# Performance work log

Measured on AMD Instinct MI355X. Metric: run time of the kernel, lower is better.

## Reference

```python
import jax, jax.numpy as jnp
import numpy as np

DIM = 1024
NUM_HEADS = 16
HEAD_DIM = DIM // NUM_HEADS
B, L = 4, 2048


def setup_inputs() -> dict:
    key = jax.random.key(0)
    ks = jax.random.split(key, 9)
    s = 0.02
    return {
        "x": jax.random.normal(ks[0], (B, L, DIM), jnp.float32),
        "Wq": jax.random.normal(ks[1], (DIM, DIM), jnp.float32) * s,
        "bq": jax.random.normal(ks[2], (DIM,), jnp.float32) * s,
        "Wk": jax.random.normal(ks[3], (DIM, DIM), jnp.float32) * s,
        "bk": jax.random.normal(ks[4], (DIM,), jnp.float32) * s,
        "Wv": jax.random.normal(ks[5], (DIM, DIM), jnp.float32) * s,
        "bv": jax.random.normal(ks[6], (DIM,), jnp.float32) * s,
        "Wo": jax.random.normal(ks[7], (DIM, DIM), jnp.float32) * s,
        "bo": jax.random.normal(ks[8], (DIM,), jnp.float32) * s,
    }


def _alibi_bias_causal(seq_len, dtype):
    # slopes m_h = 2^(-8h/H), h = 1..H
    h = jnp.arange(1, NUM_HEADS + 1, dtype=jnp.float32)
    slopes = jnp.power(2.0, -8.0 * h / NUM_HEADS)  # [H]
    pos = jnp.arange(seq_len, dtype=jnp.float32)
    rel = jnp.abs(pos[:, None] - pos[None, :])  # [L, L]
    bias = -slopes[:, None, None] * rel[None, :, :]  # [H, L, L]
    causal = pos[:, None] >= pos[None, :]  # lower-triangular True
    bias = jnp.where(causal[None, :, :], bias, -jnp.inf)
    return bias.astype(dtype)  # [H, L, L]


def reference(x, Wq, bq, Wk, bk, Wv, bv, Wo, bo):
    b, l, d = x.shape
    # torch Linear: y = x @ W.T + b
    q = (jnp.einsum('bld,ed->ble', x, Wq) + bq).reshape(b, l, NUM_HEADS, HEAD_DIM).transpose(0, 2, 1, 3)
    k = (jnp.einsum('bld,ed->ble', x, Wk) + bk).reshape(b, l, NUM_HEADS, HEAD_DIM).transpose(0, 2, 1, 3)
    v = (jnp.einsum('bld,ed->ble', x, Wv) + bv).reshape(b, l, NUM_HEADS, HEAD_DIM).transpose(0, 2, 1, 3)

    scale = 1.0 / np.sqrt(HEAD_DIM)
    scores = jnp.einsum('bhqd,bhkd->bhqk', q, k) * scale  # [B,H,L,L]
    scores = scores + _alibi_bias_causal(l, scores.dtype)[None]  # causal -inf inside bias
    attn = jax.nn.softmax(scores, axis=-1)
    out = jnp.einsum('bhqk,bhkd->bhqd', attn, v)  # [B,H,L,hd]
    out = out.transpose(0, 2, 1, 3).reshape(b, l, d)
    return jnp.einsum('bld,ed->ble', out, Wo) + bo
```

## Files before the change

kernel.cpp:

```cpp
#include <hip/hip_runtime.h>
#include <hip/hip_bf16.h>

typedef __bf16 bf16;
typedef __attribute__((ext_vector_type(4))) __bf16 bf16x4;
typedef __attribute__((ext_vector_type(8))) __bf16 bf16x8;
typedef __attribute__((ext_vector_type(4))) float f32x4;

#define MFMA16(a,b,c) __builtin_amdgcn_mfma_f32_16x16x32_bf16((a),(b),(c),0,0,0)

constexpr int BSZ = 4, SEQ = 2048, DIM = 1024, NH = 16, HD = 64;
constexpr long SZ    = (long)BSZ * SEQ * DIM;
constexpr long BSLOT = (long)SEQ * DIM;
constexpr long WSZ   = (long)DIM * DIM;

__device__ inline bf16x8 ld8(const bf16* p) { return *(const bf16x8*)p; }
__device__ inline bf16x8 ld8(const float* p) {
    f32x4 a = *(const f32x4*)p;
    f32x4 b = *(const f32x4*)(p + 4);
    bf16x8 r;
    r[0] = (bf16)a[0]; r[1] = (bf16)a[1]; r[2] = (bf16)a[2]; r[3] = (bf16)a[3];
    r[4] = (bf16)b[0]; r[5] = (bf16)b[1]; r[6] = (bf16)b[2]; r[7] = (bf16)b[3];
    return r;
}

__device__ inline void async16(const bf16* g, bf16* l) {
    __builtin_amdgcn_global_load_lds(
        (const __attribute__((address_space(1))) unsigned int*)g,
        (__attribute__((address_space(3))) unsigned int*)l,
        16, 0, 0);
}

__global__ __launch_bounds__(256) void cvt1(const float* __restrict__ s,
                                            bf16* __restrict__ d, long n) {
    const long i = ((long)blockIdx.x * 256 + threadIdx.x) * 8;
    if (i < n) *(bf16x8*)(d + i) = ld8(s + i);
}
__global__ __launch_bounds__(256) void cvt4(
    const float* __restrict__ x,  const float* __restrict__ Wq,
    const float* __restrict__ Wk, const float* __restrict__ Wv,
    bf16* __restrict__ xb, bf16* __restrict__ wqb,
    bf16* __restrict__ wkb, bf16* __restrict__ wvb) {
    const long i = ((long)blockIdx.x * 256 + threadIdx.x) * 8;
    const float* s; bf16* d; long off;
    if (i < SZ) { s = x; d = xb; off = i; }
    else {
        const long j = i - SZ;
        const int w = (int)(j >> 20);
        off = j & (WSZ - 1);
        s = (w == 0) ? Wq : (w == 1) ? Wk : Wv;
        d = (w == 0) ? wqb : (w == 1) ? wkb : wvb;
    }
    *(bf16x8*)(d + off) = ld8(s + off);
}

template <typename CT>
__global__ __launch_bounds__(256) void gemm_bb(
    const bf16* __restrict__ A,
    const bf16* __restrict__ W0, const bf16* __restrict__ W1, const bf16* __restrict__ W2,
    const float* __restrict__ b0, const float* __restrict__ b1, const float* __restrict__ b2,
    CT* __restrict__ C0, CT* __restrict__ C1, CT* __restrict__ C2,
    int M, int N, int K)
{
    const int z = blockIdx.z;
    const bf16* W     = (z == 0) ? W0 : ((z == 1) ? W1 : W2);
    const float* bias = (z == 0) ? b0 : ((z == 1) ? b1 : b2);
    CT* C             = (z == 0) ? C0 : ((z == 1) ? C1 : C2);

    __shared__ __align__(16) bf16 As[2][128][32];
    __shared__ __align__(16) bf16 Bs[2][128][32];

    const int tid  = threadIdx.x;
    const int lane = tid & 63;
    const int wave = tid >> 6;
    const int l15  = lane & 15;
    const int quad = lane >> 4;

    const int m0 = blockIdx.x * 128;
    const int n0 = blockIdx.y * 128;
    const int wm = (wave >> 1) * 64;
    const int wn = (wave & 1) * 64;

    f32x4 acc[4][4];
#pragma unroll
    for (int i = 0; i < 4; i++)
#pragma unroll
        for (int j = 0; j < 4; j++) acc[i][j] = f32x4{0.f, 0.f, 0.f, 0.f};

    const int r1 = tid >> 2,         c1 = (tid & 3) * 8;
    const int r2 = (tid + 256) >> 2, c2 = ((tid + 256) & 3) * 8;

    async16(A + (long)(m0 + r1) * K + c1, &As[0][r1][c1]);
    async16(A + (long)(m0 + r2) * K + c2, &As[0][r2][c2]);
    async16(W + (long)(n0 + r1) * K + c1, &Bs[0][r1][c1]);
    async16(W + (long)(n0 + r2) * K + c2, &Bs[0][r2][c2]);
    __syncthreads();

    const int NT = K >> 5;
    for (int t = 0; t < NT; t++) {
        const int cur = t & 1;
        if (t + 1 < NT) {
            const int k0 = (t + 1) * 32;
            async16(A + (long)(m0 + r1) * K + k0 + c1, &As[cur ^ 1][r1][c1]);
            async16(A + (long)(m0 + r2) * K + k0 + c2, &As[cur ^ 1][r2][c2]);
            async16(W + (long)(n0 + r1) * K + k0 + c1, &Bs[cur ^ 1][r1][c1]);
            async16(W + (long)(n0 + r2) * K + k0 + c2, &Bs[cur ^ 1][r2][c2]);
        }

        bf16x8 af[4], bfr[4];
#pragma unroll
        for (int t4 = 0; t4 < 4; t4++) {
            af[t4]  = *(const bf16x8*)&As[cur][wm + t4 * 16 + l15][quad * 8];
            bfr[t4] = *(const bf16x8*)&Bs[cur][wn + t4 * 16 + l15][quad * 8];
        }
#pragma unroll
        for (int i = 0; i < 4; i++)
#pragma unroll
            for (int j = 0; j < 4; j++)
                acc[i][j] = MFMA16(af[i], bfr[j], acc[i][j]);

        __syncthreads();
    }

#pragma unroll
    for (int j = 0; j < 4; j++) {
        const float bv = bias[n0 + wn + j * 16 + l15];
        const long col = n0 + wn + j * 16 + l15;
#pragma unroll
        for (int i = 0; i < 4; i++) {
            const long row = m0 + wm + i * 16 + quad * 4;
#pragma unroll
            for (int r = 0; r < 4; r++)
                C[(row + r) * N + col] = (CT)(acc[i][j][r] + bv);
        }
    }
}

template <typename AT, typename CT>
__global__ __launch_bounds__(256) void gemm_bt(
    const AT* __restrict__ A,
    const float* __restrict__ W0, const float* __restrict__ W1, const float* __restrict__ W2,
    const float* __restrict__ b0, const float* __restrict__ b1, const float* __restrict__ b2,
    CT* __restrict__ C0, CT* __restrict__ C1, CT* __restrict__ C2,
    int M, int N, int K)
{
    const int z = blockIdx.z;
    const float* W    = (z == 0) ? W0 : ((z == 1) ? W1 : W2);
    const float* bias = (z == 0) ? b0 : ((z == 1) ? b1 : b2);
    CT* C             = (z == 0) ? C0 : ((z == 1) ? C1 : C2);

    __shared__ __align__(16) bf16 As[128][32];
    __shared__ __align__(16) bf16 Bs[128][32];

    const int tid  = threadIdx.x;
    const int lane = tid & 63;
    const int wave = tid >> 6;
    const int l15  = lane & 15;
    const int quad = lane >> 4;

    const int m0 = blockIdx.x * 128;
    const int n0 = blockIdx.y * 128;
    const int wm = (wave >> 1) * 64;
    const int wn = (wave & 1) * 64;

    f32x4 acc[4][4];
#pragma unroll
    for (int i = 0; i < 4; i++)
#pragma unroll
        for (int j = 0; j < 4; j++) acc[i][j] = f32x4{0.f, 0.f, 0.f, 0.f};

    const int r1 = tid >> 2,         c1 = (tid & 3) * 8;
    const int r2 = (tid + 256) >> 2, c2 = ((tid + 256) & 3) * 8;

    for (int k0 = 0; k0 < K; k0 += 32) {
        __syncthreads();
        *(bf16x8*)&As[r1][c1] = ld8(A + (long)(m0 + r1) * K + k0 + c1);
        *(bf16x8*)&As[r2][c2] = ld8(A + (long)(m0 + r2) * K + k0 + c2);
        *(bf16x8*)&Bs[r1][c1] = ld8(W + (long)(n0 + r1) * K + k0 + c1);
        *(bf16x8*)&Bs[r2][c2] = ld8(W + (long)(n0 + r2) * K + k0 + c2);
        __syncthreads();

        bf16x8 af[4], bfr[4];
#pragma unroll
        for (int t = 0; t < 4; t++) {
            af[t]  = *(const bf16x8*)&As[wm + t * 16 + l15][quad * 8];
            bfr[t] = *(const bf16x8*)&Bs[wn + t * 16 + l15][quad * 8];
        }
#pragma unroll
        for (int i = 0; i < 4; i++)
#pragma unroll
            for (int j = 0; j < 4; j++)
                acc[i][j] = MFMA16(af[i], bfr[j], acc[i][j]);
    }

#pragma unroll
    for (int j = 0; j < 4; j++) {
        const float bv = bias[n0 + wn + j * 16 + l15];
        const long col = n0 + wn + j * 16 + l15;
#pragma unroll
        for (int i = 0; i < 4; i++) {
            const long row = m0 + wm + i * 16 + quad * 4;
#pragma unroll
            for (int r = 0; r < 4; r++)
                C[(row + r) * N + col] = (CT)(acc[i][j][r] + bv);
        }
    }
}

__global__ __launch_bounds__(256, 4) void attn(
    const bf16* __restrict__ Kw, const bf16* __restrict__ Vw,
    bf16* __restrict__ QOw)
{
    const int z  = blockIdx.y;
    const int bh = blockIdx.x;
    const int b = bh >> 4, h = bh & 15;
    const int qtA = z, qtB = 31 - z;
    const int tid = threadIdx.x, wave = tid >> 6, lane = tid & 63;
    const int l15 = lane & 15, quad = lane >> 4;

    __shared__ __align__(16) bf16 Vt[2][64][72];
    __shared__ __align__(16) bf16 Kt[2][64][64];
    __shared__ __align__(16) bf16 Pl[2][4][16][72];

    const long base = (long)b * SEQ * DIM + h * HD;
    const int q0A = qtA * 64 + wave * 16;
    const int q0B = qtB * 64 + wave * 16;

    bf16x8 qA0, qA1, qB0, qB1;
    {
        const bf16* pA = QOw + base + (long)(q0A + l15) * DIM + quad * 8;
        qA0 = *(const bf16x8*)pA; qA1 = *(const bf16x8*)(pA + 32);
        const bf16* pB = QOw + base + (long)(q0B + l15) * DIM + quad * 8;
        qB0 = *(const bf16x8*)pB; qB1 = *(const bf16x8*)(pB + 32);
    }

    constexpr float LOG2E = 1.4426950408889634f;
    const float slope = exp2f(-0.5f * (float)(h + 1));
    const float c1 = 0.125f * LOG2E;
    const float ns = slope * LOG2E;
    const float MC = 16.0f * LOG2E;

    float lrA = 0.f, lrB = 0.f;
    f32x4 oA[4], oB[4];
#pragma unroll
    for (int d = 0; d < 4; d++) { oA[d] = f32x4{0,0,0,0}; oB[d] = f32x4{0,0,0,0}; }

    const int sk0 = tid >> 3,         sd0 = (tid & 7) * 8;
    const int sk1 = (tid + 256) >> 3, sd1 = ((tid + 256) & 7) * 8;
    const int vc0 = sk0 ^ sd0,        vc1 = sk1 ^ sd1;

    auto stageK = [&](int kt, int bi) {
#pragma unroll
        for (int t = 0; t < 2; t++) {
            const int s = tid + 256 * t;
            const int r = s >> 3, u = s & 7;
            const int gc = (u ^ (r & 7)) * 8;
            async16(Kw + base + (long)(kt * 64 + r) * DIM + gc, &Kt[bi][r][u * 8]);
        }
    };

    stageK(0, 0);
    {
        bf16x8 v0 = *(const bf16x8*)(Vw + base + (long)sk0 * DIM + sd0);
        bf16x8 v1 = *(const bf16x8*)(Vw + base + (long)sk1 * DIM + sd1);
#pragma unroll
        for (int i = 0; i < 8; i++) Vt[0][sd0 + i][vc0] = v0[i];
#pragma unroll
        for (int i = 0; i < 8; i++) Vt[0][sd1 + i][vc1] = v1[i];
    }
    __syncthreads();

    const int klq = quad * 4;
    const int qlB = wave * 16 + l15;
    const int kc0 = (quad ^ (l15 & 7)) * 8;

    for (int kt = 0; kt <= qtB; kt++) {
        const int bi = kt & 1;
        const bool more = (kt < qtB);
        const bool dual = (kt <= qtA);

        bf16x8 vn0, vn1;
        if (more) {
            stageK(kt + 1, bi ^ 1);
            vn0 = *(const bf16x8*)(Vw + base + (long)((kt + 1) * 64 + sk0) * DIM + sd0);
            vn1 = *(const bf16x8*)(Vw + base + (long)((kt + 1) * 64 + sk1) * DIM + sd1);
        }

        f32x4 sB[4], sA[4];
#pragma unroll
        for (int nt = 0; nt < 4; nt++) {
            const int row = nt * 16 + l15;
            bf16x8 k0 = *(const bf16x8*)&Kt[bi][row][kc0];
            bf16x8 k1 = *(const bf16x8*)&Kt[bi][row][kc0 ^ 32];
            f32x4 a = f32x4{0,0,0,0};
            a = MFMA16(k0, qB0, a); a = MFMA16(k1, qB1, a);
            sB[nt] = a;
            if (dual) {
                f32x4 c = f32x4{0,0,0,0};
                c = MFMA16(k0, qA0, c); c = MFMA16(k1, qA1, c);
                sA[nt] = c;
            }
        }

        {
            const float t0 = fmaf(ns, (float)(kt * 64 + klq - q0B - l15), -MC);
            const bool diag = (kt == qtB);
#pragma unroll
            for (int nt = 0; nt < 4; nt++) {
                const float bn = fmaf(ns, (float)(16 * nt), t0);
                bf16x4 p4;
#pragma unroll
                for (int r = 0; r < 4; r++) {
                    float arg = fmaf(sB[nt][r], c1, fmaf(ns, (float)r, bn));
                    if (diag && (nt * 16 + klq + r > qlB)) arg = -1e30f;
                    const float p = exp2f(arg);
                    lrB += p;
                    p4[r] = (bf16)p;
                }
                *(bf16x4*)&Pl[0][wave][l15][nt * 16 + klq] = p4;
            }
        }

        if (dual) {
            const float t0 = fmaf(ns, (float)(kt * 64 + klq - q0A - l15), -MC);
            const bool diag = (kt == qtA);
#pragma unroll
            for (int nt = 0; nt < 4; nt++) {
                const float bn = fmaf(ns, (float)(16 * nt), t0);
                bf16x4 p4;
#pragma unroll
                for (int r = 0; r < 4; r++) {
                    float arg = fmaf(sA[nt][r], c1, fmaf(ns, (float)r, bn));
                    if (diag && (nt * 16 + klq + r > qlB)) arg = -1e30f;
                    const float p = exp2f(arg);
                    lrA += p;
                    p4[r] = (bf16)p;
                }
                *(bf16x4*)&Pl[1][wave][l15][nt * 16 + klq] = p4;
            }
        } else if (more) {
#pragma unroll
            for (int i = 0; i < 8; i++) Vt[bi ^ 1][sd0 + i][vc0] = vn0[i];
#pragma unroll
            for (int i = 0; i < 8; i++) Vt[bi ^ 1][sd1 + i][vc1] = vn1[i];
        }

        {
            bf16x8 p0 = *(const bf16x8*)&Pl[0][wave][l15][quad * 8];
            bf16x8 p1 = *(const bf16x8*)&Pl[0][wave][l15][32 + quad * 8];
#pragma unroll
            for (int dt = 0; dt < 4; dt++) {
                const int d = dt * 16 + l15;
                const int c0 = (quad * 8) ^ (d & 56);
                bf16x8 v0 = *(const bf16x8*)&Vt[bi][d][c0];
                bf16x8 v1 = *(const bf16x8*)&Vt[bi][d][c0 ^ 32];
                oB[dt] = MFMA16(p0, v0, oB[dt]);
                oB[dt] = MFMA16(p1, v1, oB[dt]);
            }
        }

        if (dual) {
            bf16x8 p0 = *(const bf16x8*)&Pl[1][wave][l15][quad * 8];
            bf16x8 p1 = *(const bf16x8*)&Pl[1][wave][l15][32 + quad * 8];
#pragma unroll
            for (int dt = 0; dt < 4; dt++) {
                const int d = dt * 16 + l15;
                const int c0 = (quad * 8) ^ (d & 56);
                bf16x8 v0 = *(const bf16x8*)&Vt[bi][d][c0];
                bf16x8 v1 = *(const bf16x8*)&Vt[bi][d][c0 ^ 32];
                oA[dt] = MFMA16(p0, v0, oA[dt]);
                oA[dt] = MFMA16(p1, v1, oA[dt]);
            }
#pragma unroll
            for (int i = 0; i < 8; i++) Vt[bi ^ 1][sd0 + i][vc0] = vn0[i];
#pragma unroll
            for (int i = 0; i < 8; i++) Vt[bi ^ 1][sd1 + i][vc1] = vn1[i];
        }
        __syncthreads();
    }

    lrB += __shfl_xor(lrB, 16, 64); lrB += __shfl_xor(lrB, 32, 64);
    lrA += __shfl_xor(lrA, 16, 64); lrA += __shfl_xor(lrA, 32, 64);
#pragma unroll
    for (int r = 0; r < 4; r++) {
        const float ivB = 1.0f / __shfl(lrB, quad * 4 + r, 64);
        const float ivA = 1.0f / __shfl(lrA, quad * 4 + r, 64);
        const long rwB = q0B + quad * 4 + r;
        const long rwA = q0A + quad * 4 + r;
#pragma unroll
        for (int dt = 0; dt < 4; dt++) {
            QOw[base + rwB * DIM + dt * 16 + l15] = (bf16)(oB[dt][r] * ivB);
            QOw[base + rwA * DIM + dt * 16 + l15] = (bf16)(oA[dt][r] * ivA);
        }
    }
}

extern "C" void kernel_launch(void* const* d_in, const int* in_sizes, int n_in,
                              void* d_out, int out_size, void* d_ws, size_t ws_size,
                              hipStream_t stream)
{
    const float* x  = (const float*)d_in[0];
    const float* Wq = (const float*)d_in[1];
    const float* bq = (const float*)d_in[2];
    const float* Wk = (const float*)d_in[3];
    const float* bk = (const float*)d_in[4];
    const float* Wv = (const float*)d_in[5];
    const float* bv = (const float*)d_in[6];
    const float* Wo = (const float*)d_in[7];
    const float* bo = (const float*)d_in[8];
    float* out = (float*)d_out;

    dim3 blk(256, 1, 1);

    if (ws_size >= (size_t)SZ * sizeof(bf16)) {
        bf16* xb  = (bf16*)d_out;
        bf16* Wqb = xb + SZ;
        bf16* Wkb = Wqb + WSZ;
        bf16* Wvb = Wkb + WSZ;
        bf16* Qb  = (bf16*)d_ws;
        bf16* Kb  = (bf16*)d_in[0];
        bf16* Vb  = Kb + SZ;
        bf16* Wob = Kb;

        cvt4<<<dim3(5632, 1, 1), blk, 0, stream>>>(x, Wq, Wk, Wv, xb, Wqb, Wkb, Wvb);

        dim3 g1(64, 8, 3);
        gemm_bb<bf16><<<g1, blk, 0, stream>>>(xb, Wqb, Wkb, Wvb, bq, bk, bv,
                                              Qb, Kb, Vb, BSZ * SEQ, DIM, DIM);
        dim3 g2(BSZ * NH, 16, 1);
        attn<<<g2, blk, 0, stream>>>(Kb, Vb, Qb);

        cvt1<<<dim3(512, 1, 1), blk, 0, stream>>>(Wo, Wob, WSZ);

        dim3 g3(64, 8, 1);
        gemm_bb<float><<<g3, blk, 0, stream>>>(Qb, Wob, Wob, Wob, bo, bo, bo,
                                               out, out, out, BSZ * SEQ, DIM, DIM);
    } else {
        bf16* outB = (bf16*)d_out;
        float* xm = const_cast<float*>(x);
        bf16* x0a = (bf16*)xm;
        bf16* x0b = x0a + BSLOT;
        bf16* x1a = (bf16*)(xm + BSLOT);

        bf16* Qs[4] = { outB + 2 * BSLOT, x0a, x0a, x0a };
        bf16* Ks[4] = { outB + 3 * BSLOT, x0b, x0b, x0b };
        bf16* Vs[4] = { outB + 4 * BSLOT, outB + 6 * BSLOT, x1a, x1a };

        dim3 gqkv(SEQ / 128, DIM / 128, 3);
        dim3 gattn(NH, 16, 1);
        dim3 gproj(SEQ / 128, DIM / 128, 1);

        for (int b = 0; b < 4; b++) {
            gemm_bt<float, bf16><<<gqkv, blk, 0, stream>>>(x + b * BSLOT, Wq, Wk, Wv,
                                                           bq, bk, bv,
                                                           Qs[b], Ks[b], Vs[b], SEQ, DIM, DIM);
            attn<<<gattn, blk, 0, stream>>>(Ks[b], Vs[b], Qs[b]);
            gemm_bt<bf16, float><<<gproj, blk, 0, stream>>>(Qs[b], Wo, Wo, Wo, bo, bo, bo,
                                                            out + b * BSLOT, out + b * BSLOT,
                                                            out + b * BSLOT, SEQ, DIM, DIM);
        }
    }
}
```

Measured before the change: 285.4 us.

## Single-buffer V and P tiles in attention, fold Wo conversion into first cast kernel

The attention kernel drops the double-buffered V tile and the second P staging buffer. Each branch now computes its P tile and immediately runs the PV MFMAs, and the next V tile is written after an extra barrier. This cuts LDS use per block, which may allow more resident blocks, at the cost of an additional __syncthreads per iteration and less overlap of V staging with compute. Separately, when the workspace is large enough, Wo is converted to bf16 together with x/Wq/Wk/Wv in one launch, removing the separate cvt1 launch.

```diff
diff --git a/kernel.cpp b/kernel.cpp
--- a/kernel.cpp
+++ b/kernel.cpp
@@ -52,6 +52,25 @@
     }
     *(bf16x8*)(d + off) = ld8(s + off);
 }
+__global__ __launch_bounds__(256) void cvt5(
+    const float* __restrict__ x,  const float* __restrict__ Wq,
+    const float* __restrict__ Wk, const float* __restrict__ Wv,
+    const float* __restrict__ Wo,
+    bf16* __restrict__ xb, bf16* __restrict__ wqb,
+    bf16* __restrict__ wkb, bf16* __restrict__ wvb,
+    bf16* __restrict__ wob) {
+    const long i = ((long)blockIdx.x * 256 + threadIdx.x) * 8;
+    const float* s; bf16* d; long off;
+    if (i < SZ) { s = x; d = xb; off = i; }
+    else {
+        const long j = i - SZ;
+        const int w = (int)(j >> 20);
+        off = j & (WSZ - 1);
+        s = (w == 0) ? Wq : (w == 1) ? Wk : (w == 2) ? Wv : Wo;
+        d = (w == 0) ? wqb : (w == 1) ? wkb : (w == 2) ? wvb : wob;
+    }
+    *(bf16x8*)(d + off) = ld8(s + off);
+}
 
 template <typename CT>
 __global__ __launch_bounds__(256) void gemm_bb(
@@ -217,9 +236,9 @@
     const int tid = threadIdx.x, wave = tid >> 6, lane = tid & 63;
     const int l15 = lane & 15, quad = lane >> 4;
 
-    __shared__ __align__(16) bf16 Vt[2][64][72];
+    __shared__ __align__(16) bf16 Vt[64][72];
     __shared__ __align__(16) bf16 Kt[2][64][64];
-    __shared__ __align__(16) bf16 Pl[2][4][16][72];
+    __shared__ __align__(16) bf16 Pl[4][16][72];
 
     const long base = (long)b * SEQ * DIM + h * HD;
     const int q0A = qtA * 64 + wave * 16;
@@ -263,9 +282,9 @@
         bf16x8 v0 = *(const bf16x8*)(Vw + base + (long)sk0 * DIM + sd0);
         bf16x8 v1 = *(const bf16x8*)(Vw + base + (long)sk1 * DIM + sd1);
 #pragma unroll
-        for (int i = 0; i < 8; i++) Vt[0][sd0 + i][vc0] = v0[i];
-#pragma unroll
-        for (int i = 0; i < 8; i++) Vt[0][sd1 + i][vc1] = v1[i];
+        for (int i = 0; i < 8; i++) Vt[sd0 + i][vc0] = v0[i];
+#pragma unroll
+        for (int i = 0; i < 8; i++) Vt[sd1 + i][vc1] = v1[i];
     }
     __syncthreads();
 
@@ -316,7 +335,21 @@
                     lrB += p;
                     p4[r] = (bf16)p;
                 }
-                *(bf16x4*)&Pl[0][wave][l15][nt * 16 + klq] = p4;
+                *(bf16x4*)&Pl[wave][l15][nt * 16 + klq] = p4;
+            }
+        }
+
+        {
+            bf16x8 p0 = *(const bf16x8*)&Pl[wave][l15][quad * 8];
+            bf16x8 p1 = *(const bf16x8*)&Pl[wave][l15][32 + quad * 8];
+#pragma unroll
+            for (int dt = 0; dt < 4; dt++) {
+                const int d = dt * 16 + l15;
+                const int c0 = (quad * 8) ^ (d & 56);
+                bf16x8 v0 = *(const bf16x8*)&Vt[d][c0];
+                bf16x8 v1 = *(const bf16x8*)&Vt[d][c0 ^ 32];
+                oB[dt] = MFMA16(p0, v0, oB[dt]);
+                oB[dt] = MFMA16(p1, v1, oB[dt]);
             }
         }
 
@@ -335,47 +368,29 @@
                     lrA += p;
                     p4[r] = (bf16)p;
                 }
-                *(bf16x4*)&Pl[1][wave][l15][nt * 16 + klq] = p4;
+                *(bf16x4*)&Pl[wave][l15][nt * 16 + klq] = p4;
             }
-        } else if (more) {
-#pragma unroll
-            for (int i = 0; i < 8; i++) Vt[bi ^ 1][sd0 + i][vc0] = vn0[i];
-#pragma unroll
-            for (int i = 0; i < 8; i++) Vt[bi ^ 1][sd1 + i][vc1] = vn1[i];
-        }
-
-        {
-            bf16x8 p0 = *(const bf16x8*)&Pl[0][wave][l15][quad * 8];
-            bf16x8 p1 = *(const bf16x8*)&Pl[0][wave][l15][32 + quad * 8];
+            bf16x8 p0 = *(const bf16x8*)&Pl[wave][l15][quad * 8];
+            bf16x8 p1 = *(const bf16x8*)&Pl[wave][l15][32 + quad * 8];
 #pragma unroll
             for (int dt = 0; dt < 4; dt++) {
                 const int d = dt * 16 + l15;
                 const int c0 = (quad * 8) ^ (d & 56);
-                bf16x8 v0 = *(const bf16x8*)&Vt[bi][d][c0];
-                bf16x8 v1 = *(const bf16x8*)&Vt[bi][d][c0 ^ 32];
-                oB[dt] = MFMA16(p0, v0, oB[dt]);
-                oB[dt] = MFMA16(p1, v1, oB[dt]);
-            }
-        }
-
-        if (dual) {
-            bf16x8 p0 = *(const bf16x8*)&Pl[1][wave][l15][quad * 8];
-            bf16x8 p1 = *(const bf16x8*)&Pl[1][wave][l15][32 + quad * 8];
-#pragma unroll
-            for (int dt = 0; dt < 4; dt++) {
-                const int d = dt * 16 + l15;
-                const int c0 = (quad * 8) ^ (d & 56);
-                bf16x8 v0 = *(const bf16x8*)&Vt[bi][d][c0];
-                bf16x8 v1 = *(const bf16x8*)&Vt[bi][d][c0 ^ 32];
+                bf16x8 v0 = *(const bf16x8*)&Vt[d][c0];
+                bf16x8 v1 = *(const bf16x8*)&Vt[d][c0 ^ 32];
                 oA[dt] = MFMA16(p0, v0, oA[dt]);
                 oA[dt] = MFMA16(p1, v1, oA[dt]);
             }
-#pragma unroll
-            for (int i = 0; i < 8; i++) Vt[bi ^ 1][sd0 + i][vc0] = vn0[i];
-#pragma unroll
-            for (int i = 0; i < 8; i++) Vt[bi ^ 1][sd1 + i][vc1] = vn1[i];
-        }
+        }
+
         __syncthreads();
+        if (more) {
+#pragma unroll
+            for (int i = 0; i < 8; i++) Vt[sd0 + i][vc0] = vn0[i];
+#pragma unroll
+            for (int i = 0; i < 8; i++) Vt[sd1 + i][vc1] = vn1[i];
+            __syncthreads();
+        }
     }
 
     lrB += __shfl_xor(lrB, 16, 64); lrB += __shfl_xor(lrB, 32, 64);
@@ -419,9 +434,17 @@
         bf16* Qb  = (bf16*)d_ws;
         bf16* Kb  = (bf16*)d_in[0];
         bf16* Vb  = Kb + SZ;
-        bf16* Wob = Kb;
-
-        cvt4<<<dim3(5632, 1, 1), blk, 0, stream>>>(x, Wq, Wk, Wv, xb, Wqb, Wkb, Wvb);
+
+        const bool woWs = ws_size >= (size_t)(SZ + WSZ) * sizeof(bf16);
+        bf16* Wob = woWs ? (Qb + SZ) : Kb;
+
+        if (woWs) {
+            cvt5<<<dim3(6144, 1, 1), blk, 0, stream>>>(x, Wq, Wk, Wv, Wo,
+                                                       xb, Wqb, Wkb, Wvb, Wob);
+        } else {
+            cvt4<<<dim3(5632, 1, 1), blk, 0, stream>>>(x, Wq, Wk, Wv,
+                                                       xb, Wqb, Wkb, Wvb);
+        }
 
         dim3 g1(64, 8, 3);
         gemm_bb<bf16><<<g1, blk, 0, stream>>>(xb, Wqb, Wkb, Wvb, bq, bk, bv,
@@ -429,7 +452,8 @@
         dim3 g2(BSZ * NH, 16, 1);
         attn<<<g2, blk, 0, stream>>>(Kb, Vb, Qb);
 
-        cvt1<<<dim3(512, 1, 1), blk, 0, stream>>>(Wo, Wob, WSZ);
+        if (!woWs)
+            cvt1<<<dim3(512, 1, 1), blk, 0, stream>>>(Wo, Wob, WSZ);
 
         dim3 g3(64, 8, 1);
         gemm_bb<float><<<g3, blk, 0, stream>>>(Qb, Wob, Wob, Wob, bo, bo, bo,
```

New measurement: 279.7 us. 2.0% less time.
